# Performance work log

Hardware: AMD Instinct MI355X
Metric: run time of the kernel (lower is better)

## Reference

```python
import jax, jax.numpy as jnp
import numpy as np

STRIDE = (1, 2, 2, 1)

def setup_inputs() -> dict:
    key = jax.random.key(0)
    k1, k2 = jax.random.split(key)
    B, H, W, C = 8, 128, 128, 64
    out_flat = (H * STRIDE[1]) * (W * STRIDE[2]) * C  # 4194304
    inputs = jax.random.normal(k1, (B, H, W, C), dtype=jnp.float32)
    indices = jax.random.randint(k2, (B, H, W, C), 0, out_flat, dtype=jnp.int64)
    return {"inputs": inputs, "indices": indices}

def reference(inputs, indices):
    # Max-unpooling: scatter pooled values into a (stride_h*H, stride_w*W) map
    # using per-batch flat argmax indices. tf.scatter_nd sums duplicates -> .add
    B, H, W, C = inputs.shape
    oH, oW = H * STRIDE[1], W * STRIDE[2]
    flat_out = oH * oW * C
    pool_flat = inputs.reshape(B, H * W * C)
    ind_flat = indices.reshape(B, H * W * C)
    b = jnp.arange(B, dtype=ind_flat.dtype)[:, None]  # [B,1] batch index
    ret = jnp.zeros((B, flat_out), dtype=inputs.dtype)
    ret = ret.at[jnp.broadcast_to(b, ind_flat.shape), ind_flat].add(pool_flat)
    return ret.reshape(B, oH, oW, C)
```

## Files before the change

### kernel.cpp

```cpp
#include <hip/hip_runtime.h>


typedef unsigned int u32;
typedef float nat_f4 __attribute__((ext_vector_type(4)));
typedef u32   nat_u4 __attribute__((ext_vector_type(4)));

constexpr int N             = 1 << 23;
constexpr int NBINS         = 4096;
constexpr int BINS_PER_B    = 512;
constexpr int BIN_FLOATS    = 8192;
constexpr int CAP           = 3072;
constexpr int KA_BLOCKS     = 1024;
constexpr int PAIRS_PER_BLK = 8192;
constexpr size_t SLAB_BYTES = (size_t)NBINS * CAP * 8;
constexpr size_t WS_NEEDED  = SLAB_BYTES + (size_t)NBINS * 4;

__global__ __launch_bounds__(1024, 8) void kA_sort(const nat_u4* __restrict__ idx4,
                                                   const nat_f4* __restrict__ val4,
                                                   uint2* __restrict__ slab,
                                                   u32* __restrict__ cursor) {
    __shared__ u32 lhist[BINS_PER_B];
    __shared__ u32 lstart[BINS_PER_B];
    __shared__ u32 lbase[BINS_PER_B];
    __shared__ u32 wsum[8];
    __shared__ uint2 sorted[PAIRS_PER_BLK];

    const int tid = threadIdx.x;
    if (tid < BINS_PER_B) lhist[tid] = 0;
    __syncthreads();

    const int cb4 = blockIdx.x * (PAIRS_PER_BLK / 4);
    const u32 bb  = (u32)(blockIdx.x >> 7) << 9;

    nat_u4 ix[2];
    nat_f4 vv[2];
    u32    rr[8];
#pragma unroll
    for (int i = 0; i < 2; ++i) {
        ix[i] = __builtin_nontemporal_load(&idx4[cb4 + i * 1024 + tid]);
        vv[i] = __builtin_nontemporal_load(&val4[cb4 + i * 1024 + tid]);
    }
#pragma unroll
    for (int i = 0; i < 2; ++i)
#pragma unroll
        for (int c = 0; c < 4; ++c)
            rr[4 * i + c] = atomicAdd(&lhist[ix[i][c] >> 13], 1u);
    __syncthreads();

    if (tid < BINS_PER_B) {
        const int lane = tid & 63, w = tid >> 6;
        const u32 v = lhist[tid];
        u32 s = v;
#pragma unroll
        for (int d = 1; d < 64; d <<= 1) {
            u32 t = __shfl_up(s, d);
            if (lane >= d) s += t;
        }
        if (lane == 63) wsum[w] = s;
        __syncthreads();
        if (tid == 0) {
            u32 acc = 0;
#pragma unroll
            for (int i = 0; i < 8; ++i) { u32 t = wsum[i]; wsum[i] = acc; acc += t; }
        }
        __syncthreads();
        lstart[tid] = s - v + wsum[w];
        const u32 r8 = (v + 7u) & ~7u;
        lbase[tid] = r8 ? atomicAdd(&cursor[bb + tid], r8) : 0u;
    } else {
        __syncthreads();
        __syncthreads();
    }
    __syncthreads();

#pragma unroll
    for (int i = 0; i < 2; ++i)
#pragma unroll
        for (int c = 0; c < 4; ++c)
            sorted[lstart[ix[i][c] >> 13] + rr[4 * i + c]] =
                make_uint2(__float_as_uint(vv[i][c]), ix[i][c]);
    __syncthreads();

#pragma unroll
    for (int k = 0; k < 8; ++k) {
        int j = k * 1024 + tid;
        uint2 p = sorted[j];
        u32 b = p.y >> 13;
        u32 r = lbase[b] + ((u32)j - lstart[b]);
        if (r < (u32)CAP)
            slab[(size_t)(bb + b) * CAP + r] = make_uint2(p.x, p.y & 8191u);
    }
    if (tid < BINS_PER_B) {
        const u32 v = lhist[tid];
        const u32 r8 = (v + 7u) & ~7u;
        uint2* sb = slab + (size_t)(bb + tid) * CAP;
        for (u32 q = v; q < r8; ++q) {
            u32 r = lbase[tid] + q;
            if (r < (u32)CAP) sb[r] = make_uint2(0u, 0u);
        }
    }
}

__global__ __launch_bounds__(512) void kB_accum(const uint2* __restrict__ slab,
                                                const u32* __restrict__ cursor,
                                                float* __restrict__ out) {
    __shared__ float acc[BIN_FLOATS];
    const int bin = blockIdx.x, tid = threadIdx.x;

    nat_f4* a4 = (nat_f4*)acc;
#pragma unroll
    for (int i = 0; i < 4; ++i) a4[tid + i * 512] = (nat_f4)0.f;
    u32 cnt = cursor[bin];
    if (cnt > (u32)CAP) cnt = (u32)CAP;
    const uint4* seg4 = (const uint4*)(slab + (size_t)bin * CAP);
    __syncthreads();

    const u32 half = cnt >> 1;
    for (u32 j = tid; j < half; j += 512) {
        uint4 p = seg4[j];
        atomicAdd(&acc[p.y], __uint_as_float(p.x));
        atomicAdd(&acc[p.w], __uint_as_float(p.z));
    }
    __syncthreads();

    nat_f4* o4 = (nat_f4*)(out + ((size_t)bin << 13));
#pragma unroll
    for (int i = 0; i < 4; ++i)
        __builtin_nontemporal_store(a4[tid + i * 512], &o4[tid + i * 512]);
}

__global__ __launch_bounds__(256) void zero_out(float4* __restrict__ out) {
    int t = blockIdx.x * blockDim.x + threadIdx.x;
    out[t] = make_float4(0.f, 0.f, 0.f, 0.f);
}
__global__ __launch_bounds__(256) void scatter_atomic(const float4* __restrict__ in,
                                                      const int4* __restrict__ idx,
                                                      float* __restrict__ out) {
    int t = blockIdx.x * blockDim.x + threadIdx.x;
    float4 v = in[t];
    int4 ix = idx[t];
    float* obase = out + ((size_t)(t >> 18) << 22);
    atomicAdd(obase + ix.x, v.x);
    atomicAdd(obase + ix.y, v.y);
    atomicAdd(obase + ix.z, v.z);
    atomicAdd(obase + ix.w, v.w);
}

extern "C" void kernel_launch(void* const* d_in, const int* in_sizes, int n_in,
                              void* d_out, int out_size, void* d_ws, size_t ws_size,
                              hipStream_t stream) {
    const float4* val4 = (const float4*)d_in[0];
    const int4*   idx4 = (const int4*)d_in[1];
    float*        out  = (float*)d_out;

    if (ws_size < WS_NEEDED) {
        zero_out<<<(out_size / 4) / 256, 256, 0, stream>>>((float4*)d_out);
        scatter_atomic<<<(N / 4) / 256, 256, 0, stream>>>(val4, idx4, out);
        return;
    }

    uint2* slab   = (uint2*)d_ws;
    u32*   cursor = (u32*)((char*)d_ws + SLAB_BYTES);

    (void)hipMemsetAsync(cursor, 0, NBINS * sizeof(u32), stream);
    kA_sort <<<KA_BLOCKS, 1024, 0, stream>>>((const nat_u4*)idx4, (const nat_f4*)val4,
                                             slab, cursor);
    kB_accum<<<NBINS, 512, 0, stream>>>(slab, cursor, out);
}
```

Baseline: 256.8 us.

## Use larger 16K-float bins, drop slab padding, and use nontemporal slab traffic

Halves the number of bins to 2048, so each bin now covers 16384 output floats. The accumulate kernel runs 1024-thread blocks with a 64KB LDS accumulator. The sort kernel no longer rounds per-bin runs up to multiples of 8 with zero padding, and the accumulator handles an odd tail element explicitly. Slab stores and loads become nontemporal. The aim is fewer global cursor atomics, fewer and longer slab segments, and no padding writes, at the cost of heavier LDS use that limits occupancy and of unaligned segment starts.

```diff
diff --git a/kernel.cpp b/kernel.cpp
--- a/kernel.cpp
+++ b/kernel.cpp
@@ -4,12 +4,15 @@
 typedef unsigned int u32;
 typedef float nat_f4 __attribute__((ext_vector_type(4)));
 typedef u32   nat_u4 __attribute__((ext_vector_type(4)));
+typedef u32   nat_u2 __attribute__((ext_vector_type(2)));
 
 constexpr int N             = 1 << 23;
-constexpr int NBINS         = 4096;
-constexpr int BINS_PER_B    = 512;
-constexpr int BIN_FLOATS    = 8192;
-constexpr int CAP           = 3072;
+constexpr int BINS_PER_B    = 256;
+constexpr int NBINS         = 2048;
+constexpr int BIN_FLOATS    = 16384;
+constexpr int BIN_SHIFT     = 14;
+constexpr u32 BIN_MASK      = 16383u;
+constexpr int CAP           = 5120;
 constexpr int KA_BLOCKS     = 1024;
 constexpr int PAIRS_PER_BLK = 8192;
 constexpr size_t SLAB_BYTES = (size_t)NBINS * CAP * 8;
@@ -17,12 +20,12 @@
 
 __global__ __launch_bounds__(1024, 8) void kA_sort(const nat_u4* __restrict__ idx4,
                                                    const nat_f4* __restrict__ val4,
-                                                   uint2* __restrict__ slab,
+                                                   nat_u2* __restrict__ slab,
                                                    u32* __restrict__ cursor) {
     __shared__ u32 lhist[BINS_PER_B];
     __shared__ u32 lstart[BINS_PER_B];
     __shared__ u32 lbase[BINS_PER_B];
-    __shared__ u32 wsum[8];
+    __shared__ u32 wsum[4];
     __shared__ uint2 sorted[PAIRS_PER_BLK];
 
     const int tid = threadIdx.x;
@@ -30,7 +33,7 @@
     __syncthreads();
 
     const int cb4 = blockIdx.x * (PAIRS_PER_BLK / 4);
-    const u32 bb  = (u32)(blockIdx.x >> 7) << 9;
+    const u32 bb  = (u32)(blockIdx.x >> 7) << 8;
 
     nat_u4 ix[2];
     nat_f4 vv[2];
@@ -44,7 +47,7 @@
     for (int i = 0; i < 2; ++i)
 #pragma unroll
         for (int c = 0; c < 4; ++c)
-            rr[4 * i + c] = atomicAdd(&lhist[ix[i][c] >> 13], 1u);
+            rr[4 * i + c] = atomicAdd(&lhist[ix[i][c] >> BIN_SHIFT], 1u);
     __syncthreads();
 
     if (tid < BINS_PER_B) {
@@ -61,12 +64,11 @@
         if (tid == 0) {
             u32 acc = 0;
 #pragma unroll
-            for (int i = 0; i < 8; ++i) { u32 t = wsum[i]; wsum[i] = acc; acc += t; }
+            for (int i = 0; i < 4; ++i) { u32 t = wsum[i]; wsum[i] = acc; acc += t; }
         }
         __syncthreads();
         lstart[tid] = s - v + wsum[w];
-        const u32 r8 = (v + 7u) & ~7u;
-        lbase[tid] = r8 ? atomicAdd(&cursor[bb + tid], r8) : 0u;
+        lbase[tid]  = v ? atomicAdd(&cursor[bb + tid], v) : 0u;
     } else {
         __syncthreads();
         __syncthreads();
@@ -77,7 +79,7 @@
     for (int i = 0; i < 2; ++i)
 #pragma unroll
         for (int c = 0; c < 4; ++c)
-            sorted[lstart[ix[i][c] >> 13] + rr[4 * i + c]] =
+            sorted[lstart[ix[i][c] >> BIN_SHIFT] + rr[4 * i + c]] =
                 make_uint2(__float_as_uint(vv[i][c]), ix[i][c]);
     __syncthreads();
 
@@ -85,48 +87,46 @@
     for (int k = 0; k < 8; ++k) {
         int j = k * 1024 + tid;
         uint2 p = sorted[j];
-        u32 b = p.y >> 13;
+        u32 b = p.y >> BIN_SHIFT;
         u32 r = lbase[b] + ((u32)j - lstart[b]);
-        if (r < (u32)CAP)
-            slab[(size_t)(bb + b) * CAP + r] = make_uint2(p.x, p.y & 8191u);
-    }
-    if (tid < BINS_PER_B) {
-        const u32 v = lhist[tid];
-        const u32 r8 = (v + 7u) & ~7u;
-        uint2* sb = slab + (size_t)(bb + tid) * CAP;
-        for (u32 q = v; q < r8; ++q) {
-            u32 r = lbase[tid] + q;
-            if (r < (u32)CAP) sb[r] = make_uint2(0u, 0u);
+        if (r < (u32)CAP) {
+            nat_u2 q = {p.x, p.y & BIN_MASK};
+            __builtin_nontemporal_store(q, &slab[(size_t)(bb + b) * CAP + r]);
         }
     }
 }
 
-__global__ __launch_bounds__(512) void kB_accum(const uint2* __restrict__ slab,
-                                                const u32* __restrict__ cursor,
-                                                float* __restrict__ out) {
+__global__ __launch_bounds__(1024, 2) void kB_accum(const nat_u4* __restrict__ slab4,
+                                                    const u32* __restrict__ cursor,
+                                                    float* __restrict__ out) {
     __shared__ float acc[BIN_FLOATS];
     const int bin = blockIdx.x, tid = threadIdx.x;
 
     nat_f4* a4 = (nat_f4*)acc;
 #pragma unroll
-    for (int i = 0; i < 4; ++i) a4[tid + i * 512] = (nat_f4)0.f;
+    for (int i = 0; i < 4; ++i) a4[tid + i * 1024] = (nat_f4)0.f;
     u32 cnt = cursor[bin];
     if (cnt > (u32)CAP) cnt = (u32)CAP;
-    const uint4* seg4 = (const uint4*)(slab + (size_t)bin * CAP);
+    const nat_u4* seg4 = slab4 + (size_t)bin * (CAP / 2);
     __syncthreads();
 
     const u32 half = cnt >> 1;
-    for (u32 j = tid; j < half; j += 512) {
-        uint4 p = seg4[j];
+    for (u32 j = tid; j < half; j += 1024) {
+        nat_u4 p = __builtin_nontemporal_load(&seg4[j]);
         atomicAdd(&acc[p.y], __uint_as_float(p.x));
         atomicAdd(&acc[p.w], __uint_as_float(p.z));
     }
+    if (tid == 0 && (cnt & 1u)) {
+        const nat_u2* seg2 = (const nat_u2*)seg4;
+        nat_u2 p = __builtin_nontemporal_load(&seg2[cnt - 1]);
+        atomicAdd(&acc[p.y], __uint_as_float(p.x));
+    }
     __syncthreads();
 
-    nat_f4* o4 = (nat_f4*)(out + ((size_t)bin << 13));
+    nat_f4* o4 = (nat_f4*)(out + ((size_t)bin << BIN_SHIFT));
 #pragma unroll
     for (int i = 0; i < 4; ++i)
-        __builtin_nontemporal_store(a4[tid + i * 512], &o4[tid + i * 512]);
+        __builtin_nontemporal_store(a4[tid + i * 1024], &o4[tid + i * 1024]);
 }
 
 __global__ __launch_bounds__(256) void zero_out(float4* __restrict__ out) {
@@ -159,11 +159,11 @@
         return;
     }
 
-    uint2* slab   = (uint2*)d_ws;
-    u32*   cursor = (u32*)((char*)d_ws + SLAB_BYTES);
+    nat_u2* slab   = (nat_u2*)d_ws;
+    u32*    cursor = (u32*)((char*)d_ws + SLAB_BYTES);
 
     (void)hipMemsetAsync(cursor, 0, NBINS * sizeof(u32), stream);
     kA_sort <<<KA_BLOCKS, 1024, 0, stream>>>((const nat_u4*)idx4, (const nat_f4*)val4,
                                              slab, cursor);
-    kB_accum<<<NBINS, 512, 0, stream>>>(slab, cursor, out);
+    kB_accum<<<NBINS, 1024, 0, stream>>>((const nat_u4*)d_ws, cursor, out);
 }
```

New measurement: 246.7 us. -4.0%, faster.
